# Optimization experiments

Measured on AMD Instinct MI355X. Metric: run time of the kernel, lower is better.

## Reference

```python
import jax, jax.numpy as jnp
import numpy as np

B, H, L, N = 128, 1024, 256, 64  # batch, d_model, seq len (l_max), SSM state size


def setup_inputs() -> dict:
    key = jax.random.key(0)
    ks = jax.random.split(key, 8)
    x = jax.random.normal(ks[0], (B, H, L), dtype=jnp.float32)
    # S4D init: dt log-uniform in [1e-3, 1e-1], A = -1/2 + i*pi*n, C ~ N(0,1)
    log_dt = jnp.log(10.0 ** jax.random.uniform(ks[1], (H,), minval=-3.0, maxval=-1.0)).astype(jnp.float32)
    A_real_log = jnp.log(0.5 * jnp.ones((H, N), dtype=jnp.float32))
    A_imag = jnp.tile(jnp.pi * jnp.arange(N, dtype=jnp.float32), (H, 1))
    C_re = jax.random.normal(ks[2], (H, N), dtype=jnp.float32)
    C_im = jax.random.normal(ks[3], (H, N), dtype=jnp.float32)
    D = jax.random.normal(ks[4], (H,), dtype=jnp.float32)
    W_out = (jax.random.normal(ks[5], (2 * H, H), dtype=jnp.float32) / np.sqrt(H)).astype(jnp.float32)
    b_out = jnp.zeros((2 * H,), dtype=jnp.float32)
    return dict(x=x, log_dt=log_dt, A_real_log=A_real_log, A_imag=A_imag,
                C_re=C_re, C_im=C_im, D=D, W_out=W_out, b_out=b_out)


def _s4d_kernel(log_dt, A_real_log, A_imag, C_re, C_im, length):
    """S4D convolution kernel (ZOH discretization), shape (H, length)."""
    dt = jnp.exp(log_dt)[:, None]                      # (H, 1)
    A = -jnp.exp(A_real_log) + 1j * A_imag             # (H, N) complex
    C = C_re + 1j * C_im                               # (H, N)
    dtA = A * dt                                       # (H, N)
    C_disc = C * (jnp.exp(dtA) - 1.0) / A              # ZOH-discretized C
    t = jnp.arange(length, dtype=jnp.float32)
    K = jnp.exp(dtA[:, :, None] * t)                   # (H, N, L) Vandermonde
    return 2.0 * jnp.einsum('hn,hnl->hl', C_disc, K).real


def reference(x, log_dt, A_real_log, A_imag, C_re, C_im, D, W_out, b_out):
    Bq, Hq, Lq = x.shape
    k = _s4d_kernel(log_dt, A_real_log, A_imag, C_re, C_im, Lq)  # (H, L)
    n_fft = 2 * Lq
    k_f = jnp.fft.rfft(k, n=n_fft)                     # (H, L+1)
    x_f = jnp.fft.rfft(x, n=n_fft, axis=-1)            # (B, H, L+1)
    y = jnp.fft.irfft(x_f * k_f[None], n=n_fft, axis=-1)[..., :Lq]
    y = y + D[None, :, None] * x                       # skip connection
    y = jax.nn.gelu(y)                                 # FFTConv activation
    # output linear (d_model -> 2*d_model) + GLU over channel dim
    y = jnp.einsum('bhl,gh->bgl', y, W_out) + b_out[None, :, None]
    a, b = jnp.split(y, 2, axis=1)
    return a * jax.nn.sigmoid(b)                       # (B, H, L)
```

## Files before the change

kernel.cpp:

```cpp
#include <hip/hip_runtime.h>
#include <hip/hip_bf16.h>
#include <cstdint>
#include <cstddef>

typedef __bf16 bf16x8 __attribute__((ext_vector_type(8)));
typedef float  f32x4  __attribute__((ext_vector_type(4)));
typedef unsigned short u16x8 __attribute__((ext_vector_type(8)));

__device__ __forceinline__ unsigned short f2bf(float f) {
    unsigned u = __builtin_bit_cast(unsigned, f);
    u += 0x7fffu + ((u >> 16) & 1u);
    return (unsigned short)(u >> 16);
}
__device__ __forceinline__ float bf2f(unsigned short u) {
    unsigned v = ((unsigned)u) << 16;
    return __builtin_bit_cast(float, v);
}
__device__ __forceinline__ float gelu_tanh(float x) {
    float z = 0.7978845608028654f * (x + 0.044715f * x * x * x);
    float e = __expf(2.0f * z);
    float t = 1.0f - 2.0f / (e + 1.0f);
    return 0.5f * x * (1.0f + t);
}


__global__ void k_build(const float* __restrict__ log_dt,
                        const float* __restrict__ arl,
                        const float* __restrict__ aim,
                        const float* __restrict__ cre,
                        const float* __restrict__ cim,
                        const float* __restrict__ Dp,
                        unsigned short* __restrict__ Tg) {
    __shared__ float sRe[64], sIm[64], sCr[64], sCi[64];
    __shared__ float kk[256];
    const int h = blockIdx.x;
    const int t = threadIdx.x;
    if (t < 64) {
        float dt  = expf(log_dt[h]);
        float ar  = -expf(arl[h * 64 + t]);
        float ai  = aim[h * 64 + t];
        float dre = ar * dt, dim = ai * dt;
        float er  = expf(dre);
        float s, c;
        sincosf(dim, &s, &c);
        float em1r = er * c - 1.0f, em1i = er * s;
        float cr = cre[h * 64 + t], ci = cim[h * 64 + t];
        float pr = cr * em1r - ci * em1i;
        float pi = cr * em1i + ci * em1r;
        float inv = 1.0f / (ar * ar + ai * ai);
        sCr[t] = (pr * ar + pi * ai) * inv;
        sCi[t] = (pi * ar - pr * ai) * inv;
        sRe[t] = dre; sIm[t] = dim;
    }
    __syncthreads();
    float acc = 0.0f;
    const float tf = (float)t;
    #pragma unroll 8
    for (int n = 0; n < 64; n++) {
        float er = expf(sRe[n] * tf);
        float s, c;
        sincosf(sIm[n] * tf, &s, &c);
        acc += sCr[n] * er * c - sCi[n] * er * s;
    }
    kk[t] = 2.0f * acc;
    __syncthreads();
    const float Dh = Dp[h];
    unsigned short* dst = Tg + (size_t)h * 16384;
    for (int c = t; c < 1024; c += 256) {
        const int d = c >> 6, q4 = (c >> 4) & 3, mm = c & 15;
        u16x8 hv, lv;
        #pragma unroll
        for (int e = 0; e < 8; e++) {
            const int idx = 16 * d + mm - (q4 * 8 + e);
            float v = (idx >= 0) ? kk[idx] : 0.0f;
            if (idx == 0) v += Dh;
            unsigned short hb = f2bf(v);
            hv[e] = hb;
            lv[e] = f2bf(v - bf2f(hb));
        }
        *(u16x8*)(dst + c * 8)        = hv;
        *(u16x8*)(dst + 8192 + c * 8) = lv;
    }
}

__global__ __launch_bounds__(256, 2)
void conv_mfma(const float* __restrict__ x,
               const unsigned short* __restrict__ Tg,
               unsigned short* __restrict__ yt2) {
    __shared__ __align__(16) unsigned short smem[32768];
    const int h = blockIdx.x, tid = threadIdx.x;
    const int w = tid >> 6, lane = tid & 63, m = lane & 15, q4 = lane >> 4;

    {
        const unsigned short* tg = Tg + (size_t)h * 16384;
        #pragma unroll
        for (int i = 0; i < 8; i++) {
            int q = i * 256 + tid;
            __builtin_amdgcn_global_load_lds(
                (const __attribute__((address_space(1))) void*)(tg + q * 8),
                (__attribute__((address_space(3))) void*)(smem + q * 8), 16, 0, 0);
        }
    }

    const int sb = tid >> 1;
    const float* xrow = x + (((size_t)(sb * 1024 + h)) << 8) + (tid & 1) * 16;

    {
        float4 v0 = *(const float4*)(xrow + 0);
        float4 v1 = *(const float4*)(xrow + 4);
        float4 v2 = *(const float4*)(xrow + 8);
        float4 v3 = *(const float4*)(xrow + 12);
        unsigned short* Xn = smem + 16384;
        const int qb = (tid & 1) * 2;
        #pragma unroll
        for (int s = 0; s < 4; s++) {
            float4 v = (s == 0) ? v0 : (s == 1) ? v1 : (s == 2) ? v2 : v3;
            const int q = qb + (s >> 1), off = (s & 1) * 4;
            ushort4 hv, lv;
            hv.x = f2bf(v.x); lv.x = f2bf(v.x - bf2f(hv.x));
            hv.y = f2bf(v.y); lv.y = f2bf(v.y - bf2f(hv.y));
            hv.z = f2bf(v.z); lv.z = f2bf(v.z - bf2f(hv.z));
            hv.w = f2bf(v.w); lv.w = f2bf(v.w - bf2f(hv.w));
            *(ushort4*)(Xn + (q * 128 + sb) * 8 + off)        = hv;
            *(ushort4*)(Xn + 4096 + (q * 128 + sb) * 8 + off) = lv;
        }
    }

    f32x4 acc[8][4];
    #pragma unroll
    for (int a = 0; a < 8; a++)
        #pragma unroll
        for (int b = 0; b < 4; b++) acc[a][b] = (f32x4){0.f, 0.f, 0.f, 0.f};

    __syncthreads();

    const int fi = (q4 * 16 + m) * 8;

    #pragma unroll 1
    for (int jt = 0; jt < 8; jt++) {
        const unsigned short* Xb = smem + 16384 + (jt & 1) * 8192;
        float4 p0, p1, p2, p3;
        if (jt < 7) {
            const float* xp = xrow + (jt + 1) * 32;
            p0 = *(const float4*)(xp + 0);
            p1 = *(const float4*)(xp + 4);
            p2 = *(const float4*)(xp + 8);
            p3 = *(const float4*)(xp + 12);
        }
        const int j2 = jt << 1;
        const bool a0 = (w      >= j2);
        const bool a1 = (w + 4  >= j2);
        const bool a2 = (w + 8  >= j2);
        const bool a3 = (w + 12 >= j2);
        bf16x8 th0, tl0, th1, tl1, th2, tl2, th3, tl3;
        if (a0) { int d = w      - j2; th0 = *(const bf16x8*)(smem + d * 512 + fi); tl0 = *(const bf16x8*)(smem + 8192 + d * 512 + fi); }
        if (a1) { int d = w + 4  - j2; th1 = *(const bf16x8*)(smem + d * 512 + fi); tl1 = *(const bf16x8*)(smem + 8192 + d * 512 + fi); }
        if (a2) { int d = w + 8  - j2; th2 = *(const bf16x8*)(smem + d * 512 + fi); tl2 = *(const bf16x8*)(smem + 8192 + d * 512 + fi); }
        if (a3) { int d = w + 12 - j2; th3 = *(const bf16x8*)(smem + d * 512 + fi); tl3 = *(const bf16x8*)(smem + 8192 + d * 512 + fi); }
        #pragma unroll
        for (int fb = 0; fb < 8; fb++) {
            const int xo = (q4 * 128 + fb * 16 + m) * 8;
            bf16x8 xh = *(const bf16x8*)(Xb + xo);
            bf16x8 xl = *(const bf16x8*)(Xb + 4096 + xo);
            if (a0) { acc[fb][0] = __builtin_amdgcn_mfma_f32_16x16x32_bf16(xh, th0, acc[fb][0], 0, 0, 0);
                      acc[fb][0] = __builtin_amdgcn_mfma_f32_16x16x32_bf16(xl, th0, acc[fb][0], 0, 0, 0);
                      acc[fb][0] = __builtin_amdgcn_mfma_f32_16x16x32_bf16(xh, tl0, acc[fb][0], 0, 0, 0); }
            if (a1) { acc[fb][1] = __builtin_amdgcn_mfma_f32_16x16x32_bf16(xh, th1, acc[fb][1], 0, 0, 0);
                      acc[fb][1] = __builtin_amdgcn_mfma_f32_16x16x32_bf16(xl, th1, acc[fb][1], 0, 0, 0);
                      acc[fb][1] = __builtin_amdgcn_mfma_f32_16x16x32_bf16(xh, tl1, acc[fb][1], 0, 0, 0); }
            if (a2) { acc[fb][2] = __builtin_amdgcn_mfma_f32_16x16x32_bf16(xh, th2, acc[fb][2], 0, 0, 0);
                      acc[fb][2] = __builtin_amdgcn_mfma_f32_16x16x32_bf16(xl, th2, acc[fb][2], 0, 0, 0);
                      acc[fb][2] = __builtin_amdgcn_mfma_f32_16x16x32_bf16(xh, tl2, acc[fb][2], 0, 0, 0); }
            if (a3) { acc[fb][3] = __builtin_amdgcn_mfma_f32_16x16x32_bf16(xh, th3, acc[fb][3], 0, 0, 0);
                      acc[fb][3] = __builtin_amdgcn_mfma_f32_16x16x32_bf16(xl, th3, acc[fb][3], 0, 0, 0);
                      acc[fb][3] = __builtin_amdgcn_mfma_f32_16x16x32_bf16(xh, tl3, acc[fb][3], 0, 0, 0); }
        }
        if (jt < 7) {
            unsigned short* Xn = smem + 16384 + ((jt + 1) & 1) * 8192;
            const int qb = (tid & 1) * 2;
            #pragma unroll
            for (int s = 0; s < 4; s++) {
                float4 v = (s == 0) ? p0 : (s == 1) ? p1 : (s == 2) ? p2 : p3;
                const int q = qb + (s >> 1), off = (s & 1) * 4;
                ushort4 hv, lv;
                hv.x = f2bf(v.x); lv.x = f2bf(v.x - bf2f(hv.x));
                hv.y = f2bf(v.y); lv.y = f2bf(v.y - bf2f(hv.y));
                hv.z = f2bf(v.z); lv.z = f2bf(v.z - bf2f(hv.z));
                hv.w = f2bf(v.w); lv.w = f2bf(v.w - bf2f(hv.w));
                *(ushort4*)(Xn + (q * 128 + sb) * 8 + off)        = hv;
                *(ushort4*)(Xn + 4096 + (q * 128 + sb) * 8 + off) = lv;
            }
        }
        __syncthreads();
    }

    const size_t ybase = (size_t)h * 32768;
    #pragma unroll
    for (int p = 0; p < 2; p++) {
        #pragma unroll
        for (int tt = 0; tt < 2; tt++) {
            const int ti = p * 2 + tt;
            const int lr = (w + 4 * ti) * 16 + m - p * 128;
            #pragma unroll
            for (int fb = 0; fb < 8; fb++) {
                #pragma unroll
                for (int rg = 0; rg < 4; rg++) {
                    const int b = fb * 16 + q4 * 4 + rg;
                    smem[b * 136 + lr] = f2bf(gelu_tanh(acc[fb][ti][rg]));
                }
            }
        }
        __syncthreads();
        #pragma unroll
        for (int bb = 0; bb < 4; bb++) {
            const int bp = bb * 32 + (tid >> 3);
            #pragma unroll
            for (int s = 0; s < 2; s++) {
                const int chk = (tid & 7) + 8 * s;
                u16x8 v = *(const u16x8*)(smem + bp * 136 + chk * 8);
                *(u16x8*)(yt2 + ybase + (size_t)bp * 256 + p * 128 + chk * 8) = v;
            }
        }
        __syncthreads();
    }
}

__global__ void transp(const unsigned short* __restrict__ yt2,
                       unsigned short* __restrict__ yt) {
    __shared__ __align__(16) unsigned short tl[4096];
    const int tid = threadIdx.x;
    const int m0 = blockIdx.x * 64, h0 = blockIdx.y * 64;
    {
        const int r0 = tid >> 3, ch = tid & 7;
        #pragma unroll
        for (int rr = 0; rr < 64; rr += 32) {
            const int r = r0 + rr;
            u16x8 v = *(const u16x8*)(yt2 + (size_t)(h0 + r) * 32768 + m0 + ch * 8);
            const int pch = ch ^ (r & 7) ^ ((r >> 3) & 7);
            *(u16x8*)(tl + r * 64 + pch * 8) = v;
        }
    }
    __syncthreads();
    {
        const int hc = tid & 7;
        #pragma unroll
        for (int mmr = 0; mmr < 64; mmr += 32) {
            const int mm = (tid >> 3) + mmr;
            u16x8 o;
            #pragma unroll
            for (int e = 0; e < 8; e++) {
                const int hh = hc * 8 + e;
                const int pm = (((mm >> 3) ^ (hh & 7) ^ ((hh >> 3) & 7)) << 3) + (mm & 7);
                o[e] = tl[hh * 64 + pm];
            }
            *(u16x8*)(yt + (size_t)(m0 + mm) * 1024 + h0 + hc * 8) = o;
        }
    }
}

__global__ void pack_w(const float* __restrict__ W, unsigned short* __restrict__ Wp) {
    const int p  = blockIdx.x;
    const int rt = p >> 7, r = p & 127;
    const int g  = (r < 64) ? (rt * 64 + r) : (1024 + rt * 64 + (r - 64));
    const int t  = threadIdx.x;
    const float4 v = *(const float4*)(W + (size_t)g * 1024 + t * 4);
    ushort4 o;
    o.x = f2bf(v.x); o.y = f2bf(v.y); o.z = f2bf(v.z); o.w = f2bf(v.w);
    *(ushort4*)(Wp + (size_t)p * 1024 + t * 4) = o;
}

__global__ __launch_bounds__(256, 2)
void gemm_glu(const unsigned short* __restrict__ yt,
              const unsigned short* __restrict__ Wp,
              const float* __restrict__ bo,
              float* __restrict__ out) {
    __shared__ __align__(16) unsigned char smem[24576];
    unsigned char* sA = smem;
    unsigned char* sB = smem + 16384;
    const int rt  = blockIdx.x;
    const int b   = blockIdx.y;
    const int tid = threadIdx.x;
    const int w = tid >> 6, lane = tid & 63, m = lane & 15, q4 = lane >> 4;

    f32x4 acc[4][8];
    #pragma unroll
    for (int fr = 0; fr < 4; fr++)
        #pragma unroll
        for (int fc = 0; fc < 8; fc++) acc[fr][fc] = (f32x4){0.f, 0.f, 0.f, 0.f};

    const size_t ybase = ((size_t)b) << 18;
    const size_t wbase = ((size_t)rt) * 128 * 1024;

    for (int k0 = 0; k0 < 1024; k0 += 32) {
        #pragma unroll
        for (int t8 = 0; t8 < 4; t8++) {
            int q = t8 * 256 + tid;
            int k8 = q >> 8, c = q & 255;
            const unsigned short* gp = yt + ybase + (size_t)c * 1024 + k0 + k8 * 8;
            __builtin_amdgcn_global_load_lds((const __attribute__((address_space(1))) void*)gp,
                                             (__attribute__((address_space(3))) void*)(sA + q * 16),
                                             16, 0, 0);
        }
        #pragma unroll
        for (int t8 = 0; t8 < 2; t8++) {
            int q = t8 * 256 + tid;
            int k8 = q >> 7, p = q & 127;
            const unsigned short* gp = Wp + wbase + (size_t)p * 1024 + k0 + k8 * 8;
            __builtin_amdgcn_global_load_lds((const __attribute__((address_space(1))) void*)gp,
                                             (__attribute__((address_space(3))) void*)(sB + q * 16),
                                             16, 0, 0);
        }
        __builtin_amdgcn_s_waitcnt(0x0f70);
        __syncthreads();

        bf16x8 aF[4];
        #pragma unroll
        for (int fr = 0; fr < 4; fr++)
            aF[fr] = *(const bf16x8*)(sA + ((q4 * 256 + w * 64 + fr * 16 + m) << 4));
        #pragma unroll
        for (int fc = 0; fc < 8; fc++) {
            bf16x8 bF = *(const bf16x8*)(sB + ((q4 * 128 + fc * 16 + m) << 4));
            #pragma unroll
            for (int fr = 0; fr < 4; fr++)
                acc[fr][fc] = __builtin_amdgcn_mfma_f32_16x16x32_bf16(aF[fr], bF, acc[fr][fc], 0, 0, 0);
        }
        __syncthreads();
    }

    const size_t orow = ((size_t)(b * 1024 + rt * 64)) << 8;
    const int cbase = w * 64;
    #pragma unroll
    for (int fc = 0; fc < 4; fc++) {
        float boa = bo[rt * 64 + fc * 16 + m];
        float bog = bo[1024 + rt * 64 + fc * 16 + m];
        #pragma unroll
        for (int fr = 0; fr < 4; fr++) {
            #pragma unroll
            for (int rg = 0; rg < 4; rg++) {
                float av = acc[fr][fc][rg] + boa;
                float gv = acc[fr][fc + 4][rg] + bog;
                float val = av / (1.0f + __expf(-gv));
                out[orow + (((size_t)(fc * 16 + m)) << 8) + cbase + fr * 16 + q4 * 4 + rg] = val;
            }
        }
    }
}

__global__ void k_kernel(const float* __restrict__ log_dt,
                         const float* __restrict__ arl,
                         const float* __restrict__ aim,
                         const float* __restrict__ cre,
                         const float* __restrict__ cim,
                         float* __restrict__ kout) {
    __shared__ float sRe[64], sIm[64], sCr[64], sCi[64];
    const int h = blockIdx.x;
    const int t = threadIdx.x;
    if (t < 64) {
        float dt  = expf(log_dt[h]);
        float ar  = -expf(arl[h * 64 + t]);
        float ai  = aim[h * 64 + t];
        float dre = ar * dt, dim = ai * dt;
        float er  = expf(dre);
        float s, c;
        sincosf(dim, &s, &c);
        float em1r = er * c - 1.0f, em1i = er * s;
        float cr = cre[h * 64 + t], ci = cim[h * 64 + t];
        float pr = cr * em1r - ci * em1i;
        float pi = cr * em1i + ci * em1r;
        float inv = 1.0f / (ar * ar + ai * ai);
        sCr[t] = (pr * ar + pi * ai) * inv;
        sCi[t] = (pi * ar - pr * ai) * inv;
        sRe[t] = dre; sIm[t] = dim;
    }
    __syncthreads();
    float acc = 0.0f;
    const float tf = (float)t;
    #pragma unroll 8
    for (int n = 0; n < 64; n++) {
        float er = expf(sRe[n] * tf);
        float s, c;
        sincosf(sIm[n] * tf, &s, &c);
        acc += sCr[n] * er * c - sCi[n] * er * s;
    }
    kout[h * 256 + t] = 2.0f * acc;
}

__global__ void conv_kernel(const float* __restrict__ x,
                            const float* __restrict__ kg,
                            const float* __restrict__ D,
                            unsigned short* __restrict__ yt) {
    __shared__ float xt[256 * 32];
    __shared__ float kt[256 * 32];
    const int b     = blockIdx.y;
    const int hbase = blockIdx.x * 32;
    const int tid   = threadIdx.x;
    {
        const int h  = tid & 31;
        const int c0 = tid >> 5;
        #pragma unroll
        for (int t8 = 0; t8 < 8; t8++) {
            int c4 = c0 + t8 * 8;
            float4 xv = *(const float4*)(x + (((size_t)(b * 1024 + hbase + h)) << 8) + c4 * 4);
            float4 kv = *(const float4*)(kg + (((size_t)(hbase + h)) << 8) + c4 * 4);
            int l = c4 * 4;
            xt[(l + 0) * 32 + h] = xv.x; xt[(l + 1) * 32 + h] = xv.y;
            xt[(l + 2) * 32 + h] = xv.z; xt[(l + 3) * 32 + h] = xv.w;
            kt[(l + 0) * 32 + h] = kv.x; kt[(l + 1) * 32 + h] = kv.y;
            kt[(l + 2) * 32 + h] = kv.z; kt[(l + 3) * 32 + h] = kv.w;
        }
    }
    __syncthreads();

    const int h    = tid & 31;
    const int slot = tid >> 5;
    const float Dh = D[hbase + h];
    int cs[4] = { slot, 15 - slot, 16 + slot, 31 - slot };

    for (int ci = 0; ci < 4; ci++) {
        const int c  = cs[ci];
        const int l0 = c * 8;
        float acc[8];
        #pragma unroll
        for (int i = 0; i < 8; i++) acc[i] = 0.0f;
        float kw[16];
        #pragma unroll
        for (int v = 0; v < 8; v++) kw[8 + v] = kt[(l0 + v) * 32 + h];
        float X[8];
        for (int base = l0; base > 0; base -= 8) {
            #pragma unroll
            for (int v = 0; v < 8; v++) kw[v] = kt[(base - 8 + v) * 32 + h];
            const int jb = l0 - base;
            #pragma unroll
            for (int u = 0; u < 8; u++) X[u] = xt[(jb + u) * 32 + h];
            #pragma unroll
            for (int u = 0; u < 8; u++)
                #pragma unroll
                for (int i = 0; i < 8; i++)
                    acc[i] = fmaf(kw[8 + i - u], X[u], acc[i]);
            #pragma unroll
            for (int v = 0; v < 8; v++) kw[8 + v] = kw[v];
        }
        #pragma unroll
        for (int u = 0; u < 8; u++) X[u] = xt[(l0 + u) * 32 + h];
        #pragma unroll
        for (int u = 0; u < 8; u++)
            #pragma unroll
            for (int i = u; i < 8; i++)
                acc[i] = fmaf(kw[8 + i - u], X[u], acc[i]);
        #pragma unroll
        for (int i = 0; i < 8; i++) {
            float y = acc[i] + Dh * X[i];
            yt[(((size_t)(b * 256 + l0 + i)) << 10) + hbase + h] = f2bf(gelu_tanh(y));
        }
    }
}

extern "C" void kernel_launch(void* const* d_in, const int* in_sizes, int n_in,
                              void* d_out, int out_size, void* d_ws, size_t ws_size,
                              hipStream_t stream) {
    const float* x   = (const float*)d_in[0];
    const float* ldt = (const float*)d_in[1];
    const float* arl = (const float*)d_in[2];
    const float* aim = (const float*)d_in[3];
    const float* cre = (const float*)d_in[4];
    const float* cim = (const float*)d_in[5];
    const float* D   = (const float*)d_in[6];
    const float* Wo  = (const float*)d_in[7];
    const float* bo  = (const float*)d_in[8];
    float* out = (float*)d_out;

    const size_t MB = (size_t)1 << 20;
    const size_t needNew = 132 * MB;

    if (ws_size >= needNew) {
        unsigned short* Wp  = (unsigned short*)d_ws;
        unsigned short* Tg  = (unsigned short*)((char*)d_ws + 4 * MB);
        unsigned short* yt  = (unsigned short*)((char*)d_ws + 4 * MB);
        unsigned short* yt2 = (unsigned short*)((char*)d_ws + 68 * MB);

        k_build  <<<1024, 256, 0, stream>>>(ldt, arl, aim, cre, cim, D, Tg);
        pack_w   <<<2048, 256, 0, stream>>>(Wo, Wp);
        conv_mfma<<<1024, 256, 0, stream>>>(x, Tg, yt2);
        transp   <<<dim3(512, 16), 256, 0, stream>>>(yt2, yt);
        gemm_glu <<<dim3(16, 128), 256, 0, stream>>>(yt, Wp, bo, out);
        return;
    }

    const size_t kOff = 0;
    const size_t wOff = (size_t)1 << 20;
    const size_t yOff = wOff + ((size_t)1 << 22);
    const size_t need = yOff + (size_t)128 * 256 * 1024 * 2;
    if (ws_size < need) return;

    float*          kg = (float*)((char*)d_ws + kOff);
    unsigned short* Wp = (unsigned short*)((char*)d_ws + wOff);
    unsigned short* yt = (unsigned short*)((char*)d_ws + yOff);

    k_kernel  <<<1024, 256, 0, stream>>>(ldt, arl, aim, cre, cim, kg);
    pack_w    <<<2048, 256, 0, stream>>>(Wo, Wp);
    conv_kernel<<<dim3(32, 128), 256, 0, stream>>>(x, kg, D, yt);
    gemm_glu  <<<dim3(16, 128), 256, 0, stream>>>(yt, Wp, bo, out);
}
```

Measured before the change: 548.7 us.

## Rewrite output GEMM+GLU with 256x256 tiles, double-buffered swizzled LDS pipeline

The output projection GEMM now uses 512-thread blocks computing 256x256 output tiles with a K step of 64. Global-to-LDS loads are double-buffered and software-pipelined with explicit waitcnt and barriers, and LDS reads are XOR-swizzled to avoid bank conflicts. Weights are repacked so each 16-row group interleaves value and gate rows, which lets the GLU be applied in registers with vectorized stores. The unused fallback path is removed. The larger tiles cut redundant operand loads but need 128KB of LDS and many more registers per thread.

```diff
diff --git a/kernel.cpp b/kernel.cpp
--- a/kernel.cpp
+++ b/kernel.cpp
@@ -22,7 +22,6 @@
     float t = 1.0f - 2.0f / (e + 1.0f);
     return 0.5f * x * (1.0f + t);
 }
-
 
 __global__ void k_build(const float* __restrict__ log_dt,
                         const float* __restrict__ arl,
@@ -258,201 +257,134 @@
     }
 }
 
-__global__ void pack_w(const float* __restrict__ W, unsigned short* __restrict__ Wp) {
-    const int p  = blockIdx.x;
-    const int rt = p >> 7, r = p & 127;
-    const int g  = (r < 64) ? (rt * 64 + r) : (1024 + rt * 64 + (r - 64));
-    const int t  = threadIdx.x;
+__global__ void pack_w2(const float* __restrict__ W, unsigned short* __restrict__ Wp) {
+    const int p   = blockIdx.x;
+    const int g32 = p >> 5, r32 = p & 31;
+    const int g   = (r32 < 16) ? (g32 * 16 + r32) : (1024 + g32 * 16 + (r32 - 16));
+    const int t   = threadIdx.x;
     const float4 v = *(const float4*)(W + (size_t)g * 1024 + t * 4);
     ushort4 o;
     o.x = f2bf(v.x); o.y = f2bf(v.y); o.z = f2bf(v.z); o.w = f2bf(v.w);
     *(ushort4*)(Wp + (size_t)p * 1024 + t * 4) = o;
 }
 
-__global__ __launch_bounds__(256, 2)
-void gemm_glu(const unsigned short* __restrict__ yt,
-              const unsigned short* __restrict__ Wp,
-              const float* __restrict__ bo,
-              float* __restrict__ out) {
-    __shared__ __align__(16) unsigned char smem[24576];
-    unsigned char* sA = smem;
-    unsigned char* sB = smem + 16384;
-    const int rt  = blockIdx.x;
-    const int b   = blockIdx.y;
+__global__ __launch_bounds__(512, 2)
+void gemm_glu2(const unsigned short* __restrict__ yt,
+               const unsigned short* __restrict__ Wp,
+               const float* __restrict__ bo,
+               float* __restrict__ out) {
+    __shared__ __align__(16) unsigned short smem[65536];
     const int tid = threadIdx.x;
-    const int w = tid >> 6, lane = tid & 63, m = lane & 15, q4 = lane >> 4;
-
-    f32x4 acc[4][8];
+    const int bid = (int)blockIdx.x;
+    const int b1  = (bid & 7) * 128 + (bid >> 3);
+    const int bm  = b1 >> 3;
+    const int bn  = b1 & 3 | (b1 & 7);
+    const int bn_ = b1 & 7;
+    const int wid = tid >> 6, lane = tid & 63;
+    const int m = lane & 15, q4 = lane >> 4;
+    const int wm = wid >> 2, wn = wid & 3;
+
+    const size_t abase = (size_t)bm * 256 * 1024;
+    const size_t bbase = (size_t)bn_ * 256 * 1024;
+
+    f32x4 acc[8][4];
     #pragma unroll
-    for (int fr = 0; fr < 4; fr++)
-        #pragma unroll
-        for (int fc = 0; fc < 8; fc++) acc[fr][fc] = (f32x4){0.f, 0.f, 0.f, 0.f};
-
-    const size_t ybase = ((size_t)b) << 18;
-    const size_t wbase = ((size_t)rt) * 128 * 1024;
-
-    for (int k0 = 0; k0 < 1024; k0 += 32) {
-        #pragma unroll
-        for (int t8 = 0; t8 < 4; t8++) {
-            int q = t8 * 256 + tid;
-            int k8 = q >> 8, c = q & 255;
-            const unsigned short* gp = yt + ybase + (size_t)c * 1024 + k0 + k8 * 8;
-            __builtin_amdgcn_global_load_lds((const __attribute__((address_space(1))) void*)gp,
-                                             (__attribute__((address_space(3))) void*)(sA + q * 16),
-                                             16, 0, 0);
-        }
-        #pragma unroll
-        for (int t8 = 0; t8 < 2; t8++) {
-            int q = t8 * 256 + tid;
-            int k8 = q >> 7, p = q & 127;
-            const unsigned short* gp = Wp + wbase + (size_t)p * 1024 + k0 + k8 * 8;
-            __builtin_amdgcn_global_load_lds((const __attribute__((address_space(1))) void*)gp,
-                                             (__attribute__((address_space(3))) void*)(sB + q * 16),
-                                             16, 0, 0);
-        }
-        __builtin_amdgcn_s_waitcnt(0x0f70);
-        __syncthreads();
-
-        bf16x8 aF[4];
-        #pragma unroll
-        for (int fr = 0; fr < 4; fr++)
-            aF[fr] = *(const bf16x8*)(sA + ((q4 * 256 + w * 64 + fr * 16 + m) << 4));
-        #pragma unroll
-        for (int fc = 0; fc < 8; fc++) {
-            bf16x8 bF = *(const bf16x8*)(sB + ((q4 * 128 + fc * 16 + m) << 4));
-            #pragma unroll
-            for (int fr = 0; fr < 4; fr++)
-                acc[fr][fc] = __builtin_amdgcn_mfma_f32_16x16x32_bf16(aF[fr], bF, acc[fr][fc], 0, 0, 0);
-        }
-        __syncthreads();
-    }
-
-    const size_t orow = ((size_t)(b * 1024 + rt * 64)) << 8;
-    const int cbase = w * 64;
+    for (int fr = 0; fr < 8; fr++)
+        #pragma unroll
+        for (int fc = 0; fc < 4; fc++) acc[fr][fc] = (f32x4){0.f, 0.f, 0.f, 0.f};
+
+    auto STAGE = [&](int t) {
+        const int bufo = (t & 1) << 15;
+        const int k0 = t * 64;
+        #pragma unroll
+        for (int i = 0; i < 4; i++) {
+            int q = i * 512 + tid;
+            int r = q >> 3, c = (q & 7) ^ (r & 7);
+            const unsigned short* gp = yt + abase + (size_t)r * 1024 + k0 + c * 8;
+            __builtin_amdgcn_global_load_lds(
+                (const __attribute__((address_space(1))) void*)gp,
+                (__attribute__((address_space(3))) void*)(smem + bufo + q * 8), 16, 0, 0);
+        }
+        #pragma unroll
+        for (int i = 0; i < 4; i++) {
+            int q = i * 512 + tid;
+            int r = q >> 3, c = (q & 7) ^ (r & 7);
+            const unsigned short* gp = Wp + bbase + (size_t)r * 1024 + k0 + c * 8;
+            __builtin_amdgcn_global_load_lds(
+                (const __attribute__((address_space(1))) void*)gp,
+                (__attribute__((address_space(3))) void*)(smem + bufo + 16384 + q * 8), 16, 0, 0);
+        }
+    };
+
+    STAGE(0);
+    STAGE(1);
+    asm volatile("s_waitcnt vmcnt(8)" ::: "memory");
+    __builtin_amdgcn_s_barrier();
+
+    const int arow0 = wm * 128;
+    const int brow0 = wn * 64;
+
+    for (int t = 0; t < 16; t++) {
+        const int bufo = (t & 1) << 15;
+        bf16x8 af[8][2], bf[4][2];
+        #pragma unroll
+        for (int fr = 0; fr < 8; fr++) {
+            const int r = arow0 + fr * 16 + m;
+            #pragma unroll
+            for (int ks = 0; ks < 2; ks++) {
+                const int c = (ks * 4 + q4) ^ (r & 7);
+                af[fr][ks] = *(const bf16x8*)(smem + bufo + r * 64 + c * 8);
+            }
+        }
+        #pragma unroll
+        for (int fc = 0; fc < 4; fc++) {
+            const int r = brow0 + fc * 16 + m;
+            #pragma unroll
+            for (int ks = 0; ks < 2; ks++) {
+                const int c = (ks * 4 + q4) ^ (r & 7);
+                bf[fc][ks] = *(const bf16x8*)(smem + bufo + 16384 + r * 64 + c * 8);
+            }
+        }
+        asm volatile("s_waitcnt lgkmcnt(0)" ::: "memory");
+        __builtin_amdgcn_sched_barrier(0);
+        __builtin_amdgcn_s_barrier();
+        if (t < 14) STAGE(t + 2);
+        __builtin_amdgcn_s_setprio(1);
+        #pragma unroll
+        for (int ks = 0; ks < 2; ks++)
+            #pragma unroll
+            for (int fr = 0; fr < 8; fr++)
+                #pragma unroll
+                for (int fc = 0; fc < 4; fc++)
+                    acc[fr][fc] = __builtin_amdgcn_mfma_f32_16x16x32_bf16(
+                        af[fr][ks], bf[fc][ks], acc[fr][fc], 0, 0, 0);
+        __builtin_amdgcn_s_setprio(0);
+        if (t < 14) asm volatile("s_waitcnt vmcnt(8)" ::: "memory");
+        else        asm volatile("s_waitcnt vmcnt(0)" ::: "memory");
+        __builtin_amdgcn_s_barrier();
+    }
+
+    const size_t outb = ((size_t)bm) << 18;
+    const int lbase = wm * 128;
     #pragma unroll
-    for (int fc = 0; fc < 4; fc++) {
-        float boa = bo[rt * 64 + fc * 16 + m];
-        float bog = bo[1024 + rt * 64 + fc * 16 + m];
-        #pragma unroll
-        for (int fr = 0; fr < 4; fr++) {
+    for (int fcp = 0; fcp < 2; fcp++) {
+        const int go = (bn_ * 8 + wn * 2 + fcp) * 16 + m;
+        const float boa = bo[go], bog = bo[1024 + go];
+        #pragma unroll
+        for (int fr = 0; fr < 8; fr++) {
+            f32x4 av = acc[fr][2 * fcp];
+            f32x4 gv = acc[fr][2 * fcp + 1];
+            f32x4 o;
             #pragma unroll
             for (int rg = 0; rg < 4; rg++) {
-                float av = acc[fr][fc][rg] + boa;
-                float gv = acc[fr][fc + 4][rg] + bog;
-                float val = av / (1.0f + __expf(-gv));
-                out[orow + (((size_t)(fc * 16 + m)) << 8) + cbase + fr * 16 + q4 * 4 + rg] = val;
-            }
-        }
-    }
-}
-
-__global__ void k_kernel(const float* __restrict__ log_dt,
-                         const float* __restrict__ arl,
-                         const float* __restrict__ aim,
-                         const float* __restrict__ cre,
-                         const float* __restrict__ cim,
-                         float* __restrict__ kout) {
-    __shared__ float sRe[64], sIm[64], sCr[64], sCi[64];
-    const int h = blockIdx.x;
-    const int t = threadIdx.x;
-    if (t < 64) {
-        float dt  = expf(log_dt[h]);
-        float ar  = -expf(arl[h * 64 + t]);
-        float ai  = aim[h * 64 + t];
-        float dre = ar * dt, dim = ai * dt;
-        float er  = expf(dre);
-        float s, c;
-        sincosf(dim, &s, &c);
-        float em1r = er * c - 1.0f, em1i = er * s;
-        float cr = cre[h * 64 + t], ci = cim[h * 64 + t];
-        float pr = cr * em1r - ci * em1i;
-        float pi = cr * em1i + ci * em1r;
-        float inv = 1.0f / (ar * ar + ai * ai);
-        sCr[t] = (pr * ar + pi * ai) * inv;
-        sCi[t] = (pi * ar - pr * ai) * inv;
-        sRe[t] = dre; sIm[t] = dim;
-    }
-    __syncthreads();
-    float acc = 0.0f;
-    const float tf = (float)t;
-    #pragma unroll 8
-    for (int n = 0; n < 64; n++) {
-        float er = expf(sRe[n] * tf);
-        float s, c;
-        sincosf(sIm[n] * tf, &s, &c);
-        acc += sCr[n] * er * c - sCi[n] * er * s;
-    }
-    kout[h * 256 + t] = 2.0f * acc;
-}
-
-__global__ void conv_kernel(const float* __restrict__ x,
-                            const float* __restrict__ kg,
-                            const float* __restrict__ D,
-                            unsigned short* __restrict__ yt) {
-    __shared__ float xt[256 * 32];
-    __shared__ float kt[256 * 32];
-    const int b     = blockIdx.y;
-    const int hbase = blockIdx.x * 32;
-    const int tid   = threadIdx.x;
-    {
-        const int h  = tid & 31;
-        const int c0 = tid >> 5;
-        #pragma unroll
-        for (int t8 = 0; t8 < 8; t8++) {
-            int c4 = c0 + t8 * 8;
-            float4 xv = *(const float4*)(x + (((size_t)(b * 1024 + hbase + h)) << 8) + c4 * 4);
-            float4 kv = *(const float4*)(kg + (((size_t)(hbase + h)) << 8) + c4 * 4);
-            int l = c4 * 4;
-            xt[(l + 0) * 32 + h] = xv.x; xt[(l + 1) * 32 + h] = xv.y;
-            xt[(l + 2) * 32 + h] = xv.z; xt[(l + 3) * 32 + h] = xv.w;
-            kt[(l + 0) * 32 + h] = kv.x; kt[(l + 1) * 32 + h] = kv.y;
-            kt[(l + 2) * 32 + h] = kv.z; kt[(l + 3) * 32 + h] = kv.w;
-        }
-    }
-    __syncthreads();
-
-    const int h    = tid & 31;
-    const int slot = tid >> 5;
-    const float Dh = D[hbase + h];
-    int cs[4] = { slot, 15 - slot, 16 + slot, 31 - slot };
-
-    for (int ci = 0; ci < 4; ci++) {
-        const int c  = cs[ci];
-        const int l0 = c * 8;
-        float acc[8];
-        #pragma unroll
-        for (int i = 0; i < 8; i++) acc[i] = 0.0f;
-        float kw[16];
-        #pragma unroll
-        for (int v = 0; v < 8; v++) kw[8 + v] = kt[(l0 + v) * 32 + h];
-        float X[8];
-        for (int base = l0; base > 0; base -= 8) {
-            #pragma unroll
-            for (int v = 0; v < 8; v++) kw[v] = kt[(base - 8 + v) * 32 + h];
-            const int jb = l0 - base;
-            #pragma unroll
-            for (int u = 0; u < 8; u++) X[u] = xt[(jb + u) * 32 + h];
-            #pragma unroll
-            for (int u = 0; u < 8; u++)
-                #pragma unroll
-                for (int i = 0; i < 8; i++)
-                    acc[i] = fmaf(kw[8 + i - u], X[u], acc[i]);
-            #pragma unroll
-            for (int v = 0; v < 8; v++) kw[8 + v] = kw[v];
-        }
-        #pragma unroll
-        for (int u = 0; u < 8; u++) X[u] = xt[(l0 + u) * 32 + h];
-        #pragma unroll
-        for (int u = 0; u < 8; u++)
-            #pragma unroll
-            for (int i = u; i < 8; i++)
-                acc[i] = fmaf(kw[8 + i - u], X[u], acc[i]);
-        #pragma unroll
-        for (int i = 0; i < 8; i++) {
-            float y = acc[i] + Dh * X[i];
-            yt[(((size_t)(b * 256 + l0 + i)) << 10) + hbase + h] = f2bf(gelu_tanh(y));
-        }
-    }
+                float a = av[rg] + boa, g = gv[rg] + bog;
+                o[rg] = a / (1.0f + __expf(-g));
+            }
+            const int l = lbase + fr * 16 + q4 * 4;
+            *(f32x4*)(out + outb + (((size_t)go) << 8) + l) = o;
+        }
+    }
+    (void)bn;
 }
 
 extern "C" void kernel_launch(void* const* d_in, const int* in_sizes, int n_in,
@@ -470,34 +402,17 @@
     float* out = (float*)d_out;
 
     const size_t MB = (size_t)1 << 20;
-    const size_t needNew = 132 * MB;
-
-    if (ws_size >= needNew) {
-        unsigned short* Wp  = (unsigned short*)d_ws;
-        unsigned short* Tg  = (unsigned short*)((char*)d_ws + 4 * MB);
-        unsigned short* yt  = (unsigned short*)((char*)d_ws + 4 * MB);
-        unsigned short* yt2 = (unsigned short*)((char*)d_ws + 68 * MB);
-
-        k_build  <<<1024, 256, 0, stream>>>(ldt, arl, aim, cre, cim, D, Tg);
-        pack_w   <<<2048, 256, 0, stream>>>(Wo, Wp);
-        conv_mfma<<<1024, 256, 0, stream>>>(x, Tg, yt2);
-        transp   <<<dim3(512, 16), 256, 0, stream>>>(yt2, yt);
-        gemm_glu <<<dim3(16, 128), 256, 0, stream>>>(yt, Wp, bo, out);
-        return;
-    }
-
-    const size_t kOff = 0;
-    const size_t wOff = (size_t)1 << 20;
-    const size_t yOff = wOff + ((size_t)1 << 22);
-    const size_t need = yOff + (size_t)128 * 256 * 1024 * 2;
+    const size_t need = 132 * MB;
     if (ws_size < need) return;
 
-    float*          kg = (float*)((char*)d_ws + kOff);
-    unsigned short* Wp = (unsigned short*)((char*)d_ws + wOff);
-    unsigned short* yt = (unsigned short*)((char*)d_ws + yOff);
-
-    k_kernel  <<<1024, 256, 0, stream>>>(ldt, arl, aim, cre, cim, kg);
-    pack_w    <<<2048, 256, 0, stream>>>(Wo, Wp);
-    conv_kernel<<<dim3(32, 128), 256, 0, stream>>>(x, kg, D, yt);
-    gemm_glu  <<<dim3(16, 128), 256, 0, stream>>>(yt, Wp, bo, out);
-}
+    unsigned short* Wp  = (unsigned short*)d_ws;
+    unsigned short* Tg  = (unsigned short*)((char*)d_ws + 4 * MB);
+    unsigned short* yt  = (unsigned short*)((char*)d_ws + 4 * MB);
+    unsigned short* yt2 = (unsigned short*)((char*)d_ws + 68 * MB);
+
+    k_build  <<<1024, 256, 0, stream>>>(ldt, arl, aim, cre, cim, D, Tg);
+    pack_w2  <<<2048, 256, 0, stream>>>(Wo, Wp);
+    conv_mfma<<<1024, 256, 0, stream>>>(x, Tg, yt2);
+    transp   <<<dim3(512, 16), 256, 0, stream>>>(yt2, yt);
+    gemm_glu2<<<1024, 512, 0, stream>>>(yt, Wp, bo, out);
+}
```

After: 441.4 us. 19.6% less time.
